# Kernel optimization log

Hardware: AMD Instinct MI355X
Metric: run time of the kernel (lower is better)

Reference implementation:

```python
import jax, jax.numpy as jnp
import numpy as np

K = 7          # median window size
PAD = (K - 1) // 2  # same padding with stride 1


def setup_inputs() -> dict:
    key = jax.random.key(0)
    x = jax.random.uniform(key, (8, 3, 512, 512), dtype=jnp.float32)
    return {"x": x}


def _median_pool_hardtanh(x):
    B, C, H, W = x.shape
    # reflect pad, same as F.pad(..., mode='reflect') with (pl,pr,pt,pb)=(3,3,3,3)
    xp = jnp.pad(x, ((0, 0), (0, 0), (PAD, PAD), (PAD, PAD)), mode='reflect')
    # Gather the 49 shifted views of the padded image (fixed small loop over
    # kernel offsets, vectorized over B,C,H,W). Shape: [B,C,H,W,49]
    patches = jnp.stack(
        [xp[:, :, i:i + H, j:j + W] for i in range(K) for j in range(K)],
        axis=-1,
    )
    # torch .median(dim=-1) over an odd count (49) equals the true median
    med = jnp.median(patches, axis=-1)
    # Hardtanh(min_val=0, max_val=1)
    return jnp.clip(med, 0.0, 1.0)


def reference(x):
    return _median_pool_hardtanh(x)
```

## Files before the change

### kernel.cpp

```cpp
#include <hip/hip_runtime.h>

#define DEV __device__ __forceinline__

template <int N> struct V { float v[N == 0 ? 1 : N]; };

template <int M, int N>
DEV V<M + N> mrg(V<M> a, V<N> b) {
    V<M + N> o;
    if constexpr (M == 0) {
#pragma unroll
        for (int i = 0; i < N; ++i) o.v[i] = b.v[i];
    } else if constexpr (N == 0) {
#pragma unroll
        for (int i = 0; i < M; ++i) o.v[i] = a.v[i];
    } else if constexpr (M == 1 && N == 1) {
        o.v[0] = fminf(a.v[0], b.v[0]);
        o.v[1] = fmaxf(a.v[0], b.v[0]);
    } else if constexpr ((M & 1) && (N & 1)) {
        constexpr int AE = (M + 1) / 2, AO = M / 2, BE = (N + 1) / 2, BO = N / 2;
        V<AE> ae; V<AO> ao; V<BE> be; V<BO> bo;
#pragma unroll
        for (int i = 0; i < AE; ++i) ae.v[i] = a.v[2 * i];
#pragma unroll
        for (int i = 0; i < AO; ++i) ao.v[i] = a.v[2 * i + 1];
#pragma unroll
        for (int i = 0; i < BE; ++i) be.v[i] = b.v[2 * i];
#pragma unroll
        for (int i = 0; i < BO; ++i) bo.v[i] = b.v[2 * i + 1];
        V<AE + BO> E = mrg<AE, BO>(ae, bo);
        V<AO + BE> O = mrg<AO, BE>(ao, be);
        constexpr int P = AE + BO;
#pragma unroll
        for (int i = 0; i < P; ++i) {
            o.v[2 * i] = fminf(E.v[i], O.v[i]);
            o.v[2 * i + 1] = fmaxf(E.v[i], O.v[i]);
        }
    } else {
        constexpr int AE = (M + 1) / 2, AO = M / 2, BE = (N + 1) / 2, BO = N / 2;
        V<AE> ae; V<AO> ao; V<BE> be; V<BO> bo;
#pragma unroll
        for (int i = 0; i < AE; ++i) ae.v[i] = a.v[2 * i];
#pragma unroll
        for (int i = 0; i < AO; ++i) ao.v[i] = a.v[2 * i + 1];
#pragma unroll
        for (int i = 0; i < BE; ++i) be.v[i] = b.v[2 * i];
#pragma unroll
        for (int i = 0; i < BO; ++i) bo.v[i] = b.v[2 * i + 1];
        V<AE + BE> E = mrg<AE, BE>(ae, be);
        V<AO + BO> O = mrg<AO, BO>(ao, bo);
        constexpr int CEn = AE + BE, COn = AO + BO;
        o.v[0] = E.v[0];
#pragma unroll
        for (int i = 0; i < COn; ++i) {
            if (i + 1 < CEn) {
                o.v[2 * i + 1] = fminf(O.v[i], E.v[i + 1]);
                o.v[2 * i + 2] = fmaxf(O.v[i], E.v[i + 1]);
            } else {
                o.v[2 * i + 1] = O.v[i];
            }
        }
    }
    return o;
}

DEV void ce(float& a, float& b) {
    float lo = fminf(a, b);
    b = fmaxf(a, b);
    a = lo;
}

DEV V<7> sort7(V<7> x) {
    float a = x.v[0], b = x.v[1], c = x.v[2];
    V<3> s3;
    s3.v[0] = fminf(fminf(a, b), c);
    s3.v[1] = __builtin_amdgcn_fmed3f(a, b, c);
    s3.v[2] = fmaxf(fmaxf(a, b), c);
    ce(x.v[3], x.v[4]); ce(x.v[5], x.v[6]);
    ce(x.v[3], x.v[5]); ce(x.v[4], x.v[6]); ce(x.v[4], x.v[5]);
    V<4> s4;
    s4.v[0] = x.v[3]; s4.v[1] = x.v[4]; s4.v[2] = x.v[5]; s4.v[3] = x.v[6];
    return mrg<3, 4>(s3, s4);
}

DEV float sel8(const V<42>& A, const V<7>& c) {
    float t0 = A.v[24];
    float t1 = fmaxf(A.v[23], c.v[0]);
    float t2 = fmaxf(A.v[22], c.v[1]);
    float t3 = fmaxf(A.v[21], c.v[2]);
    float t4 = fmaxf(A.v[20], c.v[3]);
    float t5 = fmaxf(A.v[19], c.v[4]);
    float t6 = fmaxf(A.v[18], c.v[5]);
    float t7 = fmaxf(A.v[17], c.v[6]);
    return fminf(fminf(fminf(t0, t1), fminf(t2, t3)),
                 fminf(fminf(t4, t5), fminf(t6, t7)));
}

static constexpr int W = 512, H = 512, PLANE = W * H;

__global__ __launch_bounds__(256) __attribute__((amdgpu_waves_per_eu(1, 7)))
void median7_hardtanh_kernel(const float* __restrict__ in,
                             float* __restrict__ out) {
    int bid = (int)blockIdx.x;
    int swz = (bid & 7) * 768 + (bid >> 3);

    int local = (int)threadIdx.x;
    int tx = local & 127;
    int ry = local >> 7;
    int chunk = (tx + 1) & 127;
    int r = swz * 2 + ry;
    int y = r & (H - 1);
    int p = r >> 9;
    const float* img = in + (size_t)p * PLANE;
    int x0 = chunk * 4;

    int rows[7];
#pragma unroll
    for (int i = 0; i < 7; ++i) {
        int t = y + i - 3;
        t = (t < 0) ? -t : t;
        t = (t > H - 1) ? 2 * (H - 1) - t : t;
        rows[i] = t << 9;
    }

    V<7> c0, c1, c2, c3, c4, c5, c6, c7, c8, c9;
    if (x0 >= 4 && x0 <= W - 8) {
#pragma unroll
        for (int i = 0; i < 7; ++i) {
            const float* rp = img + rows[i] + x0;
            float4 L = *reinterpret_cast<const float4*>(rp - 4);
            float4 C = *reinterpret_cast<const float4*>(rp);
            float4 R = *reinterpret_cast<const float4*>(rp + 4);
            c0.v[i] = L.y; c1.v[i] = L.z; c2.v[i] = L.w;
            c3.v[i] = C.x; c4.v[i] = C.y; c5.v[i] = C.z; c6.v[i] = C.w;
            c7.v[i] = R.x; c8.v[i] = R.y; c9.v[i] = R.z;
        }
    } else if (x0 == 0) {
#pragma unroll
        for (int i = 0; i < 7; ++i) {
            const float* rp = img + rows[i];
            float4 A = *reinterpret_cast<const float4*>(rp);
            float4 B = *reinterpret_cast<const float4*>(rp + 4);
            c0.v[i] = A.w; c1.v[i] = A.z; c2.v[i] = A.y;
            c3.v[i] = A.x; c4.v[i] = A.y; c5.v[i] = A.z; c6.v[i] = A.w;
            c7.v[i] = B.x; c8.v[i] = B.y; c9.v[i] = B.z;
        }
    } else {
#pragma unroll
        for (int i = 0; i < 7; ++i) {
            const float* rp = img + rows[i];
            float4 A = *reinterpret_cast<const float4*>(rp + 504);
            float4 B = *reinterpret_cast<const float4*>(rp + 508);
            c0.v[i] = A.y; c1.v[i] = A.z; c2.v[i] = A.w;
            c3.v[i] = B.x; c4.v[i] = B.y; c5.v[i] = B.z; c6.v[i] = B.w;
            c7.v[i] = B.z; c8.v[i] = B.y; c9.v[i] = B.x;
        }
    }

    c0 = sort7(c0); c1 = sort7(c1); c2 = sort7(c2); c3 = sort7(c3);
    c4 = sort7(c4); c5 = sort7(c5); c6 = sort7(c6); c7 = sort7(c7);
    c8 = sort7(c8); c9 = sort7(c9);

    V<28> Q = mrg<14, 14>(mrg<7, 7>(c3, c4), mrg<7, 7>(c5, c6));

    V<42> QP12 = mrg<28, 14>(Q, mrg<7, 7>(c1, c2));
    float m0 = sel8(QP12, c0);
    float m1 = sel8(QP12, c7);

    V<42> QP78 = mrg<28, 14>(Q, mrg<7, 7>(c7, c8));
    float m2 = sel8(QP78, c2);
    float m3 = sel8(QP78, c9);

    float4 o;
    o.x = __builtin_amdgcn_fmed3f(m0, 0.0f, 1.0f);
    o.y = __builtin_amdgcn_fmed3f(m1, 0.0f, 1.0f);
    o.z = __builtin_amdgcn_fmed3f(m2, 0.0f, 1.0f);
    o.w = __builtin_amdgcn_fmed3f(m3, 0.0f, 1.0f);
    *reinterpret_cast<float4*>(out + (size_t)r * W + x0) = o;
}

extern "C" void kernel_launch(void* const* d_in, const int* in_sizes, int n_in,
                              void* d_out, int out_size, void* d_ws, size_t ws_size,
                              hipStream_t stream) {
    const float* x = (const float*)d_in[0];
    float* outp = (float*)d_out;
    int rows_total = out_size / W;
    int blocks = rows_total / 2;
    median7_hardtanh_kernel<<<blocks, 256, 0, stream>>>(x, outp);
}
```

Measured before the change: 110.1 us.

## Compute eight output pixels per thread to share column sorts and merges

Each thread now produces eight adjacent outputs instead of four, loading 14 columns per row and sorting 14 column vectors rather than 10. The sorted columns and merges are shared across both output groups, so there is less sorting and loading per output. The block shrinks to 128 threads, with two rows interleaved across adjacent lanes. The cost is much higher register pressure (the waves-per-EU cap drops to 3), which lowers occupancy, and the stores are no longer contiguous across lanes.

```diff
diff --git a/kernel.cpp b/kernel.cpp
--- a/kernel.cpp
+++ b/kernel.cpp
@@ -97,85 +97,107 @@
 
 static constexpr int W = 512, H = 512, PLANE = W * H;
 
-__global__ __launch_bounds__(256) __attribute__((amdgpu_waves_per_eu(1, 7)))
+__global__ __launch_bounds__(128) __attribute__((amdgpu_waves_per_eu(1, 3)))
 void median7_hardtanh_kernel(const float* __restrict__ in,
                              float* __restrict__ out) {
     int bid = (int)blockIdx.x;
     int swz = (bid & 7) * 768 + (bid >> 3);
 
-    int local = (int)threadIdx.x;
-    int tx = local & 127;
-    int ry = local >> 7;
-    int chunk = (tx + 1) & 127;
-    int r = swz * 2 + ry;
+    int t = (int)threadIdx.x;
+    int rw = t & 1;
+    int cidx = ((t >> 1) + 1) & 63;
+    int r = swz * 2 + rw;
     int y = r & (H - 1);
     int p = r >> 9;
     const float* img = in + (size_t)p * PLANE;
-    int x0 = chunk * 4;
+    int x0 = cidx << 3;
 
     int rows[7];
 #pragma unroll
     for (int i = 0; i < 7; ++i) {
-        int t = y + i - 3;
-        t = (t < 0) ? -t : t;
-        t = (t > H - 1) ? 2 * (H - 1) - t : t;
-        rows[i] = t << 9;
+        int tt = y + i - 3;
+        tt = (tt < 0) ? -tt : tt;
+        tt = (tt > H - 1) ? 2 * (H - 1) - tt : tt;
+        rows[i] = tt << 9;
     }
 
-    V<7> c0, c1, c2, c3, c4, c5, c6, c7, c8, c9;
-    if (x0 >= 4 && x0 <= W - 8) {
+    V<7> c0, c1, c2, c3, c4, c5, c6, c7, c8, c9, c10, c11, c12, c13;
+#define SETCOLS(i, v0, v1, v2, v3, v4, v5, v6, v7, v8, v9, v10, v11, v12, v13) \
+    c0.v[i] = v0; c1.v[i] = v1; c2.v[i] = v2; c3.v[i] = v3; c4.v[i] = v4;       \
+    c5.v[i] = v5; c6.v[i] = v6; c7.v[i] = v7; c8.v[i] = v8; c9.v[i] = v9;       \
+    c10.v[i] = v10; c11.v[i] = v11; c12.v[i] = v12; c13.v[i] = v13;
+
+    if (cidx >= 1 && cidx <= 62) {
 #pragma unroll
         for (int i = 0; i < 7; ++i) {
             const float* rp = img + rows[i] + x0;
             float4 L = *reinterpret_cast<const float4*>(rp - 4);
-            float4 C = *reinterpret_cast<const float4*>(rp);
-            float4 R = *reinterpret_cast<const float4*>(rp + 4);
-            c0.v[i] = L.y; c1.v[i] = L.z; c2.v[i] = L.w;
-            c3.v[i] = C.x; c4.v[i] = C.y; c5.v[i] = C.z; c6.v[i] = C.w;
-            c7.v[i] = R.x; c8.v[i] = R.y; c9.v[i] = R.z;
-        }
-    } else if (x0 == 0) {
+            float4 A = *reinterpret_cast<const float4*>(rp);
+            float4 B = *reinterpret_cast<const float4*>(rp + 4);
+            float4 C = *reinterpret_cast<const float4*>(rp + 8);
+            SETCOLS(i, L.y, L.z, L.w, A.x, A.y, A.z, A.w,
+                    B.x, B.y, B.z, B.w, C.x, C.y, C.z)
+        }
+    } else if (cidx == 0) {
 #pragma unroll
         for (int i = 0; i < 7; ++i) {
             const float* rp = img + rows[i];
             float4 A = *reinterpret_cast<const float4*>(rp);
             float4 B = *reinterpret_cast<const float4*>(rp + 4);
-            c0.v[i] = A.w; c1.v[i] = A.z; c2.v[i] = A.y;
-            c3.v[i] = A.x; c4.v[i] = A.y; c5.v[i] = A.z; c6.v[i] = A.w;
-            c7.v[i] = B.x; c8.v[i] = B.y; c9.v[i] = B.z;
+            float4 C = *reinterpret_cast<const float4*>(rp + 8);
+            SETCOLS(i, A.w, A.z, A.y, A.x, A.y, A.z, A.w,
+                    B.x, B.y, B.z, B.w, C.x, C.y, C.z)
         }
     } else {
 #pragma unroll
         for (int i = 0; i < 7; ++i) {
             const float* rp = img + rows[i];
-            float4 A = *reinterpret_cast<const float4*>(rp + 504);
-            float4 B = *reinterpret_cast<const float4*>(rp + 508);
-            c0.v[i] = A.y; c1.v[i] = A.z; c2.v[i] = A.w;
-            c3.v[i] = B.x; c4.v[i] = B.y; c5.v[i] = B.z; c6.v[i] = B.w;
-            c7.v[i] = B.z; c8.v[i] = B.y; c9.v[i] = B.x;
+            float4 B = *reinterpret_cast<const float4*>(rp + 500);
+            float4 C = *reinterpret_cast<const float4*>(rp + 504);
+            float4 D = *reinterpret_cast<const float4*>(rp + 508);
+            SETCOLS(i, B.y, B.z, B.w, C.x, C.y, C.z, C.w,
+                    D.x, D.y, D.z, D.w, D.z, D.y, D.x)
         }
     }
+#undef SETCOLS
 
     c0 = sort7(c0); c1 = sort7(c1); c2 = sort7(c2); c3 = sort7(c3);
     c4 = sort7(c4); c5 = sort7(c5); c6 = sort7(c6); c7 = sort7(c7);
-    c8 = sort7(c8); c9 = sort7(c9);
-
-    V<28> Q = mrg<14, 14>(mrg<7, 7>(c3, c4), mrg<7, 7>(c5, c6));
-
-    V<42> QP12 = mrg<28, 14>(Q, mrg<7, 7>(c1, c2));
-    float m0 = sel8(QP12, c0);
-    float m1 = sel8(QP12, c7);
-
-    V<42> QP78 = mrg<28, 14>(Q, mrg<7, 7>(c7, c8));
-    float m2 = sel8(QP78, c2);
-    float m3 = sel8(QP78, c9);
-
-    float4 o;
-    o.x = __builtin_amdgcn_fmed3f(m0, 0.0f, 1.0f);
-    o.y = __builtin_amdgcn_fmed3f(m1, 0.0f, 1.0f);
-    o.z = __builtin_amdgcn_fmed3f(m2, 0.0f, 1.0f);
-    o.w = __builtin_amdgcn_fmed3f(m3, 0.0f, 1.0f);
-    *reinterpret_cast<float4*>(out + (size_t)r * W + x0) = o;
+    c8 = sort7(c8); c9 = sort7(c9); c10 = sort7(c10); c11 = sort7(c11);
+    c12 = sort7(c12); c13 = sort7(c13);
+
+    V<28> QA = mrg<14, 14>(mrg<7, 7>(c3, c4), mrg<7, 7>(c5, c6));
+    V<14> P12 = mrg<7, 7>(c1, c2);
+    V<42> QPA12 = mrg<28, 14>(QA, P12);
+    float m0 = sel8(QPA12, c0);
+    float m1 = sel8(QPA12, c7);
+    V<14> P78 = mrg<7, 7>(c7, c8);
+    V<42> QPA78 = mrg<28, 14>(QA, P78);
+    float m2 = sel8(QPA78, c2);
+    float m3 = sel8(QPA78, c9);
+
+    V<28> QB = mrg<14, 14>(mrg<7, 7>(c7, c8), mrg<7, 7>(c9, c10));
+    V<14> P56 = mrg<7, 7>(c5, c6);
+    V<42> QPB56 = mrg<28, 14>(QB, P56);
+    float m4 = sel8(QPB56, c4);
+    float m5 = sel8(QPB56, c11);
+    V<14> P1112 = mrg<7, 7>(c11, c12);
+    V<42> QPB1112 = mrg<28, 14>(QB, P1112);
+    float m6 = sel8(QPB1112, c6);
+    float m7 = sel8(QPB1112, c13);
+
+    float* op = out + (size_t)r * W + x0;
+    float4 o1, o2;
+    o1.x = __builtin_amdgcn_fmed3f(m0, 0.0f, 1.0f);
+    o1.y = __builtin_amdgcn_fmed3f(m1, 0.0f, 1.0f);
+    o1.z = __builtin_amdgcn_fmed3f(m2, 0.0f, 1.0f);
+    o1.w = __builtin_amdgcn_fmed3f(m3, 0.0f, 1.0f);
+    o2.x = __builtin_amdgcn_fmed3f(m4, 0.0f, 1.0f);
+    o2.y = __builtin_amdgcn_fmed3f(m5, 0.0f, 1.0f);
+    o2.z = __builtin_amdgcn_fmed3f(m6, 0.0f, 1.0f);
+    o2.w = __builtin_amdgcn_fmed3f(m7, 0.0f, 1.0f);
+    *reinterpret_cast<float4*>(op) = o1;
+    *reinterpret_cast<float4*>(op + 4) = o2;
 }
 
 extern "C" void kernel_launch(void* const* d_in, const int* in_sizes, int n_in,
@@ -185,5 +207,5 @@
     float* outp = (float*)d_out;
     int rows_total = out_size / W;
     int blocks = rows_total / 2;
-    median7_hardtanh_kernel<<<blocks, 256, 0, stream>>>(x, outp);
-}
+    median7_hardtanh_kernel<<<blocks, 128, 0, stream>>>(x, outp);
+}
```

Result: slower. 116.2 us (+5.5%).
